# Kernel optimization log

Hardware: AMD Instinct MI355X
Metric: run time of the kernel (lower is better)

## Reference

```python
import jax, jax.numpy as jnp
import numpy as np

NEG = -1e9


def _layer_norm(x, g, b, eps=1e-5):
    m = x.mean(-1, keepdims=True)
    v = x.var(-1, keepdims=True)
    return (x - m) / jnp.sqrt(v + eps) * g + b


def _gat(x, mask, W, a):
    # x: [B,N,Fin], W: [Fin,Fout], a: [2*Fout]
    h = x @ W                                   # [B,N,Fout]
    F = W.shape[1]
    src = h @ a[:F]                             # [B,N]
    dst = h @ a[F:]                             # [B,N]
    e = jax.nn.leaky_relu(src[:, :, None] + dst[:, None, :], 0.2)  # [B,N,N]
    e = jnp.where(mask, e, NEG)
    attn = jax.nn.softmax(e, axis=-1)
    return attn @ h, attn


def _mha(x, mask, Wq, bq, Wk, bk, Wv, bv, Wo, bo, num_heads, head_dim):
    B, N, _ = x.shape
    q = (x @ Wq + bq).reshape(B, N, num_heads, head_dim)
    k = (x @ Wk + bk).reshape(B, N, num_heads, head_dim)
    v = (x @ Wv + bv).reshape(B, N, num_heads, head_dim)
    scores = jnp.einsum('bihd,bjhd->bhij', q, k) / jnp.sqrt(jnp.asarray(head_dim, x.dtype))
    scores = jnp.where(mask[:, None, :, :], scores, NEG)
    attn = jax.nn.softmax(scores, axis=-1)      # [B,H,N,N]
    ctx = jnp.einsum('bhij,bjhd->bihd', attn, v).reshape(B, N, num_heads * head_dim)
    return ctx @ Wo + bo, attn


def setup_inputs() -> dict:
    key = jax.random.key(0)
    ks = jax.random.split(key, 32)
    B, N = 64, 400
    D, Hd, E, H = 400, 256, 128, 4
    hd = Hd // H  # 64
    s = 0.02
    x = jax.random.normal(ks[0], (B, N, D), dtype=jnp.float32)
    adj = (jax.random.uniform(ks[1], (B, N, N)) < 0.15).astype(jnp.float32)
    eye = jnp.eye(N, dtype=jnp.float32)
    adj = jnp.maximum(adj, eye[None])
    def w(k, shape):
        return jax.random.normal(k, shape, dtype=jnp.float32) * s
    return {
        'x': x, 'adj': adj,
        'Wq': w(ks[2], (D, H * hd)), 'bq': jnp.zeros(H * hd),
        'Wk': w(ks[3], (D, H * hd)), 'bk': jnp.zeros(H * hd),
        'Wv': w(ks[4], (D, H * hd)), 'bv': jnp.zeros(H * hd),
        'Wo': w(ks[5], (H * hd, D)), 'bo': jnp.zeros(D),
        'gat1_W': w(ks[6], (D, Hd)), 'gat1_a': w(ks[7], (2 * Hd,)),
        'gat2_W': w(ks[8], (Hd, Hd)), 'gat2_a': w(ks[9], (2 * Hd,)),
        'gat3_W': w(ks[10], (Hd, E)), 'gat3_a': w(ks[11], (2 * E,)),
        'res1_W': w(ks[12], (D, Hd)), 'res1_b': jnp.zeros(Hd),
        'res2_W': w(ks[13], (Hd, Hd)), 'res2_b': jnp.zeros(Hd),
        'res3_W': w(ks[14], (Hd, E)), 'res3_b': jnp.zeros(E),
        'ln1_g': jnp.ones(Hd), 'ln1_b': jnp.zeros(Hd),
        'ln2_g': jnp.ones(Hd), 'ln2_b': jnp.zeros(Hd),
        'ln3_g': jnp.ones(E), 'ln3_b': jnp.zeros(E),
    }


def reference(x, adj, Wq, bq, Wk, bk, Wv, bv, Wo, bo,
              gat1_W, gat1_a, gat2_W, gat2_a, gat3_W, gat3_a,
              res1_W, res1_b, res2_W, res2_b, res3_W, res3_b,
              ln1_g, ln1_b, ln2_g, ln2_b, ln3_g, ln3_b):
    mask = adj > 0
    # eval mode: dropout is identity
    mha_out, _ = _mha(x, mask, Wq, bq, Wk, bk, Wv, bv, Wo, bo, num_heads=4, head_dim=64)
    x = x + mha_out
    g1, attn1 = _gat(x, mask, gat1_W, gat1_a)
    x = jax.nn.elu(_layer_norm(g1 + (x @ res1_W + res1_b), ln1_g, ln1_b))
    g2, attn2 = _gat(x, mask, gat2_W, gat2_a)
    x = jax.nn.elu(_layer_norm(g2 + (x @ res2_W + res2_b), ln2_g, ln2_b))
    g3, attn3 = _gat(x, mask, gat3_W, gat3_a)
    x = _layer_norm(g3 + (x @ res3_W + res3_b), ln3_g, ln3_b)
    return x, (attn1, attn2, attn3)
```

## Files before the change

### kernel.cpp

```cpp
#include <hip/hip_runtime.h>


#define NEGBIG (-1e9f)

typedef __attribute__((ext_vector_type(8))) short bf16x8;
typedef __attribute__((ext_vector_type(4))) float f32x4;

__device__ inline unsigned short f2bf(float f) {
    unsigned u = __builtin_bit_cast(unsigned, f);
    u += 0x7fffu + ((u >> 16) & 1u);
    return (unsigned short)(u >> 16);
}
__device__ inline float bf2f(unsigned short h) {
    unsigned u = ((unsigned)h) << 16;
    return __builtin_bit_cast(float, u);
}

__device__ inline float wave_max(float v) {
#pragma unroll
    for (int off = 32; off >= 1; off >>= 1)
        v = fmaxf(v, __shfl_xor(v, off, 64));
    return v;
}
__device__ inline float wave_sum(float v) {
#pragma unroll
    for (int off = 32; off >= 1; off >>= 1)
        v += __shfl_xor(v, off, 64);
    return v;
}

__global__ void build_biases(
    float* bqkv, const float* bq, const float* bk, const float* bv,
    float* bgr1, const float* r1b, float* bgr2, const float* r2b,
    float* bgr3, const float* r3b)
{
    const int t = threadIdx.x;
    bqkv[t] = bq[t]; bqkv[256 + t] = bk[t]; bqkv[512 + t] = bv[t];
    bgr1[t] = 0.f; bgr1[256 + t] = r1b[t];
    bgr2[t] = 0.f; bgr2[256 + t] = r2b[t];
    if (t < 128) { bgr3[t] = 0.f; bgr3[128 + t] = r3b[t]; }
}

__global__ __launch_bounds__(256) void transpose_to_bf16(
    const float* __restrict__ in, unsigned short* __restrict__ out,
    int R, int C, int ldIn, long sIn, long sOut)
{
    in  += (long)blockIdx.z * sIn;
    out += (long)blockIdx.z * sOut;
    __shared__ float t[32][33];
    const int r0 = blockIdx.y * 32, c0 = blockIdx.x * 32;
    const int tid = threadIdx.x;

    const int row = tid >> 3, c4 = tid & 7;
    float4 v = make_float4(0.f, 0.f, 0.f, 0.f);
    if (r0 + row < R && c0 + c4 * 4 < C)
        v = *reinterpret_cast<const float4*>(&in[(long)(r0 + row) * ldIn + c0 + c4 * 4]);
    t[row][c4 * 4 + 0] = v.x;
    t[row][c4 * 4 + 1] = v.y;
    t[row][c4 * 4 + 2] = v.z;
    t[row][c4 * 4 + 3] = v.w;
    __syncthreads();

    const int oc = tid >> 3, r4 = tid & 7;
    if (c0 + oc < C && r0 + r4 * 4 < R) {
        ushort4 o;
        o.x = f2bf(t[r4 * 4 + 0][oc]);
        o.y = f2bf(t[r4 * 4 + 1][oc]);
        o.z = f2bf(t[r4 * 4 + 2][oc]);
        o.w = f2bf(t[r4 * 4 + 3][oc]);
        *reinterpret_cast<ushort4*>(&out[(long)(c0 + oc) * R + r0 + r4 * 4]) = o;
    }
}

template<bool BIAS, bool ACCUM, bool RESID>
__global__ __launch_bounds__(512) void gemm_mfma(
    const float* __restrict__ A, const unsigned short* __restrict__ BT,
    const float* __restrict__ bias, const float* __restrict__ resid,
    float* __restrict__ C, int M, int K, int Nc, int ldA, int ldC,
    long sA, long sBT, long sC)
{
    const int bz = blockIdx.z;
    A  += (long)bz * sA;
    BT += (long)bz * sBT;
    C  += (long)bz * sC;
    const float* Rp = RESID ? (resid + (long)bz * sC) : nullptr;

    __shared__ short As[128][40];
    __shared__ short Bs[256][40];

    const int tid = threadIdx.x;
    const int lane = tid & 63, wave = tid >> 6;
    const int wm = wave >> 2, wn = wave & 3;
    const int m0 = blockIdx.y * 128, n0 = blockIdx.x * 256;

    f32x4 acc[4][4] = {};

    const int nk = (K + 31) / 32;
    for (int kt = 0; kt < nk; ++kt) {
        const int k0 = kt * 32;
        __syncthreads();
#pragma unroll
        for (int p = 0; p < 2; ++p) {
            const int idx = tid + p * 512;
            const int row = idx >> 3, k4 = idx & 7;
            const int gm = m0 + row, gk = k0 + k4 * 4;
            float4 av = make_float4(0.f, 0.f, 0.f, 0.f);
            if (gm < M && gk < K)
                av = *reinterpret_cast<const float4*>(&A[(long)gm * ldA + gk]);
            ushort4 h4;
            h4.x = f2bf(av.x); h4.y = f2bf(av.y); h4.z = f2bf(av.z); h4.w = f2bf(av.w);
            *reinterpret_cast<ushort4*>(&As[row][k4 * 4]) = h4;
        }
#pragma unroll
        for (int p = 0; p < 2; ++p) {
            const int idx = tid + p * 512;
            const int n = idx >> 2, k8 = idx & 3;
            const int gn = n0 + n, gk = k0 + k8 * 8;
            uint4 bv = make_uint4(0u, 0u, 0u, 0u);
            if (gn < Nc && gk < K)
                bv = *reinterpret_cast<const uint4*>(&BT[(long)gn * K + gk]);
            *reinterpret_cast<uint4*>(&Bs[n][k8 * 8]) = bv;
        }
        __syncthreads();

        const int fr = lane & 15, fkb = (lane >> 4) * 8;
        bf16x8 a[4], b[4];
#pragma unroll
        for (int i = 0; i < 4; ++i)
            a[i] = *reinterpret_cast<const bf16x8*>(&As[wm * 64 + i * 16 + fr][fkb]);
#pragma unroll
        for (int j = 0; j < 4; ++j)
            b[j] = *reinterpret_cast<const bf16x8*>(&Bs[wn * 64 + j * 16 + fr][fkb]);
#pragma unroll
        for (int i = 0; i < 4; ++i)
#pragma unroll
            for (int j = 0; j < 4; ++j)
                acc[i][j] = __builtin_amdgcn_mfma_f32_16x16x32_bf16(a[i], b[j], acc[i][j], 0, 0, 0);
    }

    const int fr = lane & 15, rg = lane >> 4;
#pragma unroll
    for (int i = 0; i < 4; ++i) {
#pragma unroll
        for (int j = 0; j < 4; ++j) {
#pragma unroll
            for (int r = 0; r < 4; ++r) {
                const int gm = m0 + wm * 64 + i * 16 + rg * 4 + r;
                const int gn = n0 + wn * 64 + j * 16 + fr;
                if (gm < M && gn < Nc) {
                    float v = acc[i][j][r];
                    if (BIAS)  v += bias[gn];
                    if (RESID) v += Rp[(long)gm * ldC + gn];
                    if (ACCUM) v += C[(long)gm * ldC + gn];
                    C[(long)gm * ldC + gn] = v;
                }
            }
        }
    }
}

__global__ __launch_bounds__(256) void mha_flash_mfma(
    const float* __restrict__ qkv, const float* __restrict__ adj,
    float* __restrict__ ctx, int ld)
{
    const int it = blockIdx.x, h = blockIdx.y, b = blockIdx.z;
    const int i0 = it * 64;
    const int tid = threadIdx.x;
    const int lane = tid & 63, w = tid >> 6;
    const int c = lane & 15, g = lane >> 4;

    __shared__ short Qs[64][72];
    __shared__ short Ks[64][72];
    __shared__ short Vt[64][72];
    __shared__ short Ps[64][72];
    __shared__ short Adjs[64][72];

    const long base_q = ((long)b * 400 + i0) * ld + h * 64;
#pragma unroll
    for (int p = 0; p < 4; ++p) {
        const int idx = tid + p * 256;
        const int r = idx >> 4, c4 = idx & 15;
        float4 qv = make_float4(0.f, 0.f, 0.f, 0.f);
        if (i0 + r < 400)
            qv = *reinterpret_cast<const float4*>(qkv + base_q + (long)r * ld + c4 * 4);
        ushort4 h4;
        h4.x = f2bf(qv.x); h4.y = f2bf(qv.y); h4.z = f2bf(qv.z); h4.w = f2bf(qv.w);
        *reinterpret_cast<ushort4*>(&Qs[r][c4 * 4]) = h4;
    }

    f32x4 o[4] = {};
    float m[4] = {-3e38f, -3e38f, -3e38f, -3e38f};
    float l[4] = {0.f, 0.f, 0.f, 0.f};

    for (int jt = 0; jt < 7; ++jt) {
        const int j0 = jt * 64;
        __syncthreads();

        const long base_k = ((long)b * 400 + j0) * ld + 256 + h * 64;
        const long base_v = base_k + 256;
#pragma unroll
        for (int p = 0; p < 4; ++p) {
            const int idx = tid + p * 256;
            const int r = idx >> 4, c4 = idx & 15;
            float4 kv = make_float4(0.f, 0.f, 0.f, 0.f);
            if (j0 + r < 400)
                kv = *reinterpret_cast<const float4*>(qkv + base_k + (long)r * ld + c4 * 4);
            ushort4 h4;
            h4.x = f2bf(kv.x); h4.y = f2bf(kv.y); h4.z = f2bf(kv.z); h4.w = f2bf(kv.w);
            *reinterpret_cast<ushort4*>(&Ks[r][c4 * 4]) = h4;

            float4 av = make_float4(0.f, 0.f, 0.f, 0.f);
            if (i0 + r < 400 && j0 + c4 * 4 < 400)
                av = *reinterpret_cast<const float4*>(adj + ((long)b * 400 + i0 + r) * 400 + j0 + c4 * 4);
            ushort4 mb;
            mb.x = f2bf(av.x > 0.f ? 0.f : NEGBIG);
            mb.y = f2bf(av.y > 0.f ? 0.f : NEGBIG);
            mb.z = f2bf(av.z > 0.f ? 0.f : NEGBIG);
            mb.w = f2bf(av.w > 0.f ? 0.f : NEGBIG);
            *reinterpret_cast<ushort4*>(&Adjs[r][c4 * 4]) = mb;
        }
        {
            const int j4 = tid >> 4, d4 = tid & 15;
            float vv[4][4];
#pragma unroll
            for (int t = 0; t < 4; ++t) {
                float4 vl = make_float4(0.f, 0.f, 0.f, 0.f);
                if (j0 + j4 * 4 + t < 400)
                    vl = *reinterpret_cast<const float4*>(qkv + base_v + (long)(j4 * 4 + t) * ld + d4 * 4);
                vv[t][0] = vl.x; vv[t][1] = vl.y; vv[t][2] = vl.z; vv[t][3] = vl.w;
            }
#pragma unroll
            for (int u = 0; u < 4; ++u) {
                ushort4 h4;
                h4.x = f2bf(vv[0][u]); h4.y = f2bf(vv[1][u]);
                h4.z = f2bf(vv[2][u]); h4.w = f2bf(vv[3][u]);
                *reinterpret_cast<ushort4*>(&Vt[d4 * 4 + u][j4 * 4]) = h4;
            }
        }
        __syncthreads();

        f32x4 s4[4] = {};
#pragma unroll
        for (int ks = 0; ks < 2; ++ks) {
            const bf16x8 a = *reinterpret_cast<const bf16x8*>(&Qs[w * 16 + c][ks * 32 + g * 8]);
#pragma unroll
            for (int t = 0; t < 4; ++t) {
                const bf16x8 bb = *reinterpret_cast<const bf16x8*>(&Ks[t * 16 + c][ks * 32 + g * 8]);
                s4[t] = __builtin_amdgcn_mfma_f32_16x16x32_bf16(a, bb, s4[t], 0, 0, 0);
            }
        }

        float e[4][4];
        float pmax[4];
#pragma unroll
        for (int reg = 0; reg < 4; ++reg) {
            const int qr = w * 16 + g * 4 + reg;
            float mx = -3e38f;
#pragma unroll
            for (int t = 0; t < 4; ++t) {
                const float ev = s4[t][reg] * 0.125f + bf2f((unsigned short)Adjs[qr][t * 16 + c]);
                e[t][reg] = ev;
                mx = fmaxf(mx, ev);
            }
            pmax[reg] = mx;
        }
#pragma unroll
        for (int reg = 0; reg < 4; ++reg)
#pragma unroll
            for (int off = 1; off <= 8; off <<= 1)
                pmax[reg] = fmaxf(pmax[reg], __shfl_xor(pmax[reg], off, 64));

        float al[4];
#pragma unroll
        for (int reg = 0; reg < 4; ++reg) {
            const float mn = fmaxf(m[reg], pmax[reg]);
            al[reg] = __expf(m[reg] - mn);
            m[reg] = mn;
        }

#pragma unroll
        for (int reg = 0; reg < 4; ++reg) {
            const int qr = w * 16 + g * 4 + reg;
            float psum = 0.f;
#pragma unroll
            for (int t = 0; t < 4; ++t) {
                const float p = __expf(e[t][reg] - m[reg]);
                psum += p;
                Ps[qr][t * 16 + c] = (short)f2bf(p);
            }
            l[reg] = l[reg] * al[reg] + psum;
        }

#pragma unroll
        for (int dt = 0; dt < 4; ++dt)
#pragma unroll
            for (int reg = 0; reg < 4; ++reg)
                o[dt][reg] *= al[reg];

#pragma unroll
        for (int ks = 0; ks < 2; ++ks) {
            const bf16x8 a = *reinterpret_cast<const bf16x8*>(&Ps[w * 16 + c][ks * 32 + g * 8]);
#pragma unroll
            for (int dt = 0; dt < 4; ++dt) {
                const bf16x8 bb = *reinterpret_cast<const bf16x8*>(&Vt[dt * 16 + c][ks * 32 + g * 8]);
                o[dt] = __builtin_amdgcn_mfma_f32_16x16x32_bf16(a, bb, o[dt], 0, 0, 0);
            }
        }
    }

#pragma unroll
    for (int reg = 0; reg < 4; ++reg)
#pragma unroll
        for (int off = 1; off <= 8; off <<= 1)
            l[reg] += __shfl_xor(l[reg], off, 64);

#pragma unroll
    for (int reg = 0; reg < 4; ++reg) {
        const int gi = i0 + w * 16 + g * 4 + reg;
        if (gi < 400) {
            const float inv = 1.f / l[reg];
#pragma unroll
            for (int dt = 0; dt < 4; ++dt)
                ctx[((long)b * 400 + gi) * 256 + h * 64 + dt * 16 + c] = o[dt][reg] * inv;
        }
    }
}

__global__ __launch_bounds__(256) void gat_srcdst(
    const float* __restrict__ h, const float* __restrict__ a,
    float* __restrict__ src, float* __restrict__ dst, int F, int ld)
{
    const int row = blockIdx.x * 4 + (threadIdx.x >> 6);
    const int lane = threadIdx.x & 63;
    const float* hp = h + (long)row * ld;
    float s = 0.f, d = 0.f;
    for (int f = lane; f < F; f += 64) {
        const float hv = hp[f];
        s += hv * a[f];
        d += hv * a[F + f];
    }
    s = wave_sum(s);
    d = wave_sum(d);
    if (lane == 0) { src[row] = s; dst[row] = d; }
}

__global__ __launch_bounds__(256) void gat_attn(
    const float* __restrict__ src, const float* __restrict__ dst,
    const float* __restrict__ adj, float* __restrict__ attn)
{
    const int row = blockIdx.x * 4 + (threadIdx.x >> 6);
    const int b = row / 400;
    const int lane = threadIdx.x & 63;
    const float si = src[row];
    const float* db = dst + (long)b * 400;
    const float* adjrow = adj + (long)row * 400;

    float e[7];
    float mx = -3.0e38f;
#pragma unroll
    for (int t = 0; t < 7; ++t) {
        const int j = lane + 64 * t;
        float v = -3.0e38f;
        if (j < 400) {
            v = si + db[j];
            v = (v > 0.f) ? v : 0.2f * v;
            if (!(adjrow[j] > 0.f)) v = NEGBIG;
        }
        e[t] = v;
        mx = fmaxf(mx, v);
    }
    mx = wave_max(mx);

    float p[7];
    float sum = 0.f;
#pragma unroll
    for (int t = 0; t < 7; ++t) {
        const int j = lane + 64 * t;
        if (j < 400) {
            p[t] = __expf(e[t] - mx);
            sum += p[t];
        }
    }
    sum = wave_sum(sum);
    const float inv = 1.f / sum;
#pragma unroll
    for (int t = 0; t < 7; ++t) {
        const int j = lane + 64 * t;
        if (j < 400) attn[(long)row * 400 + j] = p[t] * inv;
    }
}

template<int F, bool ELU>
__global__ __launch_bounds__(256) void ln_kernel(
    const float* __restrict__ in, int ldIn, const float* __restrict__ g,
    const float* __restrict__ b, float* __restrict__ out)
{
    const int row = blockIdx.x * 4 + (threadIdx.x >> 6);
    const int lane = threadIdx.x & 63;
    constexpr int PER = F / 64;
    const float* ip = in + (long)row * ldIn;

    float v[PER];
    float s = 0.f;
#pragma unroll
    for (int t = 0; t < PER; ++t) {
        v[t] = ip[lane + 64 * t];
        s += v[t];
    }
    s = wave_sum(s);
    const float mean = s * (1.f / F);
    float vs = 0.f;
#pragma unroll
    for (int t = 0; t < PER; ++t) {
        const float d = v[t] - mean;
        vs += d * d;
    }
    vs = wave_sum(vs);
    const float rstd = rsqrtf(vs * (1.f / F) + 1e-5f);
#pragma unroll
    for (int t = 0; t < PER; ++t) {
        const int col = lane + 64 * t;
        float y = (v[t] - mean) * rstd * g[col] + b[col];
        if (ELU) y = (y > 0.f) ? y : expm1f(y);
        out[(long)row * F + col] = y;
    }
}

extern "C" void kernel_launch(void* const* d_in, const int* in_sizes, int n_in,
                              void* d_out, int out_size, void* d_ws, size_t ws_size,
                              hipStream_t stream) {
    const float* x    = (const float*)d_in[0];
    const float* adj  = (const float*)d_in[1];
    const float* Wq   = (const float*)d_in[2];
    const float* bq   = (const float*)d_in[3];
    const float* Wk   = (const float*)d_in[4];
    const float* bk   = (const float*)d_in[5];
    const float* Wv   = (const float*)d_in[6];
    const float* bv   = (const float*)d_in[7];
    const float* Wo   = (const float*)d_in[8];
    const float* bo   = (const float*)d_in[9];
    const float* g1W  = (const float*)d_in[10];
    const float* g1a  = (const float*)d_in[11];
    const float* g2W  = (const float*)d_in[12];
    const float* g2a  = (const float*)d_in[13];
    const float* g3W  = (const float*)d_in[14];
    const float* g3a  = (const float*)d_in[15];
    const float* r1W  = (const float*)d_in[16];
    const float* r1b  = (const float*)d_in[17];
    const float* r2W  = (const float*)d_in[18];
    const float* r2b  = (const float*)d_in[19];
    const float* r3W  = (const float*)d_in[20];
    const float* r3b  = (const float*)d_in[21];
    const float* ln1g = (const float*)d_in[22];
    const float* ln1b = (const float*)d_in[23];
    const float* ln2g = (const float*)d_in[24];
    const float* ln2b = (const float*)d_in[25];
    const float* ln3g = (const float*)d_in[26];
    const float* ln3b = (const float*)d_in[27];

    float* out_x = (float*)d_out;
    float* attn1 = out_x + 3276800;
    float* attn2 = attn1 + 10240000;
    float* attn3 = attn2 + 10240000;

    float* bufA = (float*)d_ws;
    float* bufB = bufA + 6553600;
    float* bufC = bufB + 6553600;
    float* bufD = bufC + 6553600;
    float* srcb = bufD + 6553600;
    float* dstb = srcb + 25600;
    unsigned short* wT   = (unsigned short*)(dstb + 25600);
    unsigned short* wTq  = wT;
    unsigned short* wTk  = wT + 102400;
    unsigned short* wTv  = wT + 204800;
    unsigned short* wTo  = wT + 307200;
    unsigned short* wTg1 = wT + 409600;
    unsigned short* wTr1 = wT + 512000;
    unsigned short* wTg2 = wT + 614400;
    unsigned short* wTr2 = wT + 679936;
    unsigned short* wTg3 = wT + 745472;
    unsigned short* wTr3 = wT + 778240;
    float* bias0 = (float*)(wT + 811008);
    float* bqkv = bias0;
    float* bgr1 = bqkv + 768;
    float* bgr2 = bgr1 + 512;
    float* bgr3 = bgr2 + 512;

    float* qkv = bufA;
    float* ctx = bufD;
    float* xc  = attn1;
    float* hr1 = bufA;
    float* hr3 = bufA;
    unsigned short* hT = (unsigned short*)bufD;
    float* x2 = bufC;
    float* x3 = bufC;

    const dim3 b256(256), b512(512);
    const int M = 25600;

    build_biases<<<1, b256, 0, stream>>>(bqkv, bq, bk, bv, bgr1, r1b, bgr2, r2b, bgr3, r3b);
    transpose_to_bf16<<<dim3(8, 13), b256, 0, stream>>>(Wq,  wTq, 400, 256, 256, 0, 0);
    transpose_to_bf16<<<dim3(8, 13), b256, 0, stream>>>(Wk,  wTk, 400, 256, 256, 0, 0);
    transpose_to_bf16<<<dim3(8, 13), b256, 0, stream>>>(Wv,  wTv, 400, 256, 256, 0, 0);
    transpose_to_bf16<<<dim3(13, 8), b256, 0, stream>>>(Wo,  wTo, 256, 400, 400, 0, 0);
    transpose_to_bf16<<<dim3(8, 13), b256, 0, stream>>>(g1W, wTg1, 400, 256, 256, 0, 0);
    transpose_to_bf16<<<dim3(8, 13), b256, 0, stream>>>(r1W, wTr1, 400, 256, 256, 0, 0);
    transpose_to_bf16<<<dim3(8, 8),  b256, 0, stream>>>(g2W, wTg2, 256, 256, 256, 0, 0);
    transpose_to_bf16<<<dim3(8, 8),  b256, 0, stream>>>(r2W, wTr2, 256, 256, 256, 0, 0);
    transpose_to_bf16<<<dim3(4, 8),  b256, 0, stream>>>(g3W, wTg3, 256, 128, 128, 0, 0);
    transpose_to_bf16<<<dim3(4, 8),  b256, 0, stream>>>(r3W, wTr3, 256, 128, 128, 0, 0);

    gemm_mfma<true, false, false><<<dim3(3, 200), b512, 0, stream>>>(
        x, wTq, bqkv, nullptr, qkv, M, 400, 768, 400, 768, 0, 0, 0);
    mha_flash_mfma<<<dim3(7, 4, 64), b256, 0, stream>>>(qkv, adj, ctx, 768);
    gemm_mfma<true, false, true><<<dim3(2, 200), b512, 0, stream>>>(
        ctx, wTo, bo, x, xc, M, 256, 400, 256, 400, 0, 0, 0);

    gemm_mfma<true, false, false><<<dim3(2, 200), b512, 0, stream>>>(
        xc, wTg1, bgr1, nullptr, hr1, M, 400, 512, 400, 512, 0, 0, 0);
    gat_srcdst<<<dim3(6400), b256, 0, stream>>>(hr1, g1a, srcb, dstb, 256, 512);
    gat_attn<<<dim3(6400), b256, 0, stream>>>(srcb, dstb, adj, attn1);
    transpose_to_bf16<<<dim3(8, 13, 64), b256, 0, stream>>>(hr1, hT, 400, 256, 512, 204800, 102400);
    gemm_mfma<false, true, false><<<dim3(1, 4, 64), b512, 0, stream>>>(
        attn1, hT, nullptr, nullptr, hr1 + 256, 400, 400, 256, 400, 512, 160000, 102400, 204800);
    ln_kernel<256, true><<<dim3(6400), b256, 0, stream>>>(hr1 + 256, 512, ln1g, ln1b, x2);

    gemm_mfma<true, false, false><<<dim3(2, 200), b512, 0, stream>>>(
        x2, wTg2, bgr2, nullptr, hr1, M, 256, 512, 256, 512, 0, 0, 0);
    gat_srcdst<<<dim3(6400), b256, 0, stream>>>(hr1, g2a, srcb, dstb, 256, 512);
    gat_attn<<<dim3(6400), b256, 0, stream>>>(srcb, dstb, adj, attn2);
    transpose_to_bf16<<<dim3(8, 13, 64), b256, 0, stream>>>(hr1, hT, 400, 256, 512, 204800, 102400);
    gemm_mfma<false, true, false><<<dim3(1, 4, 64), b512, 0, stream>>>(
        attn2, hT, nullptr, nullptr, hr1 + 256, 400, 400, 256, 400, 512, 160000, 102400, 204800);
    ln_kernel<256, true><<<dim3(6400), b256, 0, stream>>>(hr1 + 256, 512, ln2g, ln2b, x3);

    gemm_mfma<true, false, false><<<dim3(1, 200), b512, 0, stream>>>(
        x3, wTg3, bgr3, nullptr, hr3, M, 256, 256, 256, 256, 0, 0, 0);
    gat_srcdst<<<dim3(6400), b256, 0, stream>>>(hr3, g3a, srcb, dstb, 128, 256);
    gat_attn<<<dim3(6400), b256, 0, stream>>>(srcb, dstb, adj, attn3);
    transpose_to_bf16<<<dim3(4, 13, 64), b256, 0, stream>>>(hr3, hT, 400, 128, 256, 102400, 51200);
    gemm_mfma<false, true, false><<<dim3(1, 4, 64), b512, 0, stream>>>(
        attn3, hT, nullptr, nullptr, hr3 + 128, 400, 400, 128, 400, 256, 160000, 51200, 102400);
    ln_kernel<128, false><<<dim3(6400), b256, 0, stream>>>(hr3 + 128, 256, ln3g, ln3b, out_x);
}
```

Before: 852.3 us.

## Keep inter-stage activations in bf16 and precompute a bf16 additive mask

QKV, the attention context, the post-MHA residual stream, the GAT layer inputs and a copy of each GAT attention matrix are now stored in bf16 instead of fp32. The GEMM kernel gains template paths to load bf16 A tiles directly and to write bf16 outputs. The fp32 adjacency is converted once into a bf16 additive mask (0 or -1e9), which the MHA and GAT attention kernels read instead of re-reading and comparing the fp32 adjacency each time. This is meant to cut global memory traffic and in-kernel conversion work. The costs are an extra bf16 attention write per GAT layer and lower precision for the residual stream and intermediate activations.

```diff
diff --git a/kernel.cpp b/kernel.cpp
--- a/kernel.cpp
+++ b/kernel.cpp
@@ -16,16 +16,16 @@
     return __builtin_bit_cast(float, u);
 }
 
+__device__ inline float wave_sum(float v) {
+#pragma unroll
+    for (int off = 32; off >= 1; off >>= 1)
+        v += __shfl_xor(v, off, 64);
+    return v;
+}
 __device__ inline float wave_max(float v) {
 #pragma unroll
     for (int off = 32; off >= 1; off >>= 1)
         v = fmaxf(v, __shfl_xor(v, off, 64));
-    return v;
-}
-__device__ inline float wave_sum(float v) {
-#pragma unroll
-    for (int off = 32; off >= 1; off >>= 1)
-        v += __shfl_xor(v, off, 64);
     return v;
 }
 
@@ -39,6 +39,19 @@
     bgr1[t] = 0.f; bgr1[256 + t] = r1b[t];
     bgr2[t] = 0.f; bgr2[256 + t] = r2b[t];
     if (t < 128) { bgr3[t] = 0.f; bgr3[128 + t] = r3b[t]; }
+}
+
+__global__ __launch_bounds__(256) void adj2mask(
+    const float* __restrict__ adj, unsigned short* __restrict__ mb)
+{
+    const long i = ((long)blockIdx.x * 256 + threadIdx.x) * 4;
+    const float4 a = *reinterpret_cast<const float4*>(adj + i);
+    ushort4 o;
+    o.x = f2bf(a.x > 0.f ? 0.f : NEGBIG);
+    o.y = f2bf(a.y > 0.f ? 0.f : NEGBIG);
+    o.z = f2bf(a.z > 0.f ? 0.f : NEGBIG);
+    o.w = f2bf(a.w > 0.f ? 0.f : NEGBIG);
+    *reinterpret_cast<ushort4*>(mb + i) = o;
 }
 
 __global__ __launch_bounds__(256) void transpose_to_bf16(
@@ -72,17 +85,19 @@
     }
 }
 
-template<bool BIAS, bool ACCUM, bool RESID>
+template<bool BIAS, bool ACCUM, bool RESID, bool ABHALF, bool OUTBF16>
 __global__ __launch_bounds__(512) void gemm_mfma(
-    const float* __restrict__ A, const unsigned short* __restrict__ BT,
+    const void* __restrict__ Av, const unsigned short* __restrict__ BT,
     const float* __restrict__ bias, const float* __restrict__ resid,
-    float* __restrict__ C, int M, int K, int Nc, int ldA, int ldC,
+    void* __restrict__ Cv, int M, int K, int Nc, int ldA, int ldC,
     long sA, long sBT, long sC)
 {
     const int bz = blockIdx.z;
-    A  += (long)bz * sA;
+    const float* Af = ABHALF ? nullptr : ((const float*)Av + (long)bz * sA);
+    const unsigned short* Ah = ABHALF ? ((const unsigned short*)Av + (long)bz * sA) : nullptr;
     BT += (long)bz * sBT;
-    C  += (long)bz * sC;
+    float* Cf = OUTBF16 ? nullptr : ((float*)Cv + (long)bz * sC);
+    unsigned short* Ch = OUTBF16 ? ((unsigned short*)Cv + (long)bz * sC) : nullptr;
     const float* Rp = RESID ? (resid + (long)bz * sC) : nullptr;
 
     __shared__ short As[128][40];
@@ -99,17 +114,26 @@
     for (int kt = 0; kt < nk; ++kt) {
         const int k0 = kt * 32;
         __syncthreads();
-#pragma unroll
-        for (int p = 0; p < 2; ++p) {
-            const int idx = tid + p * 512;
-            const int row = idx >> 3, k4 = idx & 7;
-            const int gm = m0 + row, gk = k0 + k4 * 4;
-            float4 av = make_float4(0.f, 0.f, 0.f, 0.f);
+        if (ABHALF) {
+            const int row = tid >> 2, k8 = tid & 3;
+            const int gm = m0 + row, gk = k0 + k8 * 8;
+            uint4 av = make_uint4(0u, 0u, 0u, 0u);
             if (gm < M && gk < K)
-                av = *reinterpret_cast<const float4*>(&A[(long)gm * ldA + gk]);
-            ushort4 h4;
-            h4.x = f2bf(av.x); h4.y = f2bf(av.y); h4.z = f2bf(av.z); h4.w = f2bf(av.w);
-            *reinterpret_cast<ushort4*>(&As[row][k4 * 4]) = h4;
+                av = *reinterpret_cast<const uint4*>(&Ah[(long)gm * ldA + gk]);
+            *reinterpret_cast<uint4*>(&As[row][k8 * 8]) = av;
+        } else {
+#pragma unroll
+            for (int p = 0; p < 2; ++p) {
+                const int idx = tid + p * 512;
+                const int row = idx >> 3, k4 = idx & 7;
+                const int gm = m0 + row, gk = k0 + k4 * 4;
+                float4 av = make_float4(0.f, 0.f, 0.f, 0.f);
+                if (gm < M && gk < K)
+                    av = *reinterpret_cast<const float4*>(&Af[(long)gm * ldA + gk]);
+                ushort4 h4;
+                h4.x = f2bf(av.x); h4.y = f2bf(av.y); h4.z = f2bf(av.z); h4.w = f2bf(av.w);
+                *reinterpret_cast<ushort4*>(&As[row][k4 * 4]) = h4;
+            }
         }
 #pragma unroll
         for (int p = 0; p < 2; ++p) {
@@ -151,8 +175,12 @@
                     float v = acc[i][j][r];
                     if (BIAS)  v += bias[gn];
                     if (RESID) v += Rp[(long)gm * ldC + gn];
-                    if (ACCUM) v += C[(long)gm * ldC + gn];
-                    C[(long)gm * ldC + gn] = v;
+                    if (OUTBF16) {
+                        Ch[(long)gm * ldC + gn] = f2bf(v);
+                    } else {
+                        if (ACCUM) v += Cf[(long)gm * ldC + gn];
+                        Cf[(long)gm * ldC + gn] = v;
+                    }
                 }
             }
         }
@@ -160,14 +188,15 @@
 }
 
 __global__ __launch_bounds__(256) void mha_flash_mfma(
-    const float* __restrict__ qkv, const float* __restrict__ adj,
-    float* __restrict__ ctx, int ld)
+    const unsigned short* __restrict__ qkv, const unsigned short* __restrict__ mask,
+    unsigned short* __restrict__ ctx, int ld)
 {
     const int it = blockIdx.x, h = blockIdx.y, b = blockIdx.z;
     const int i0 = it * 64;
     const int tid = threadIdx.x;
     const int lane = tid & 63, w = tid >> 6;
     const int c = lane & 15, g = lane >> 4;
+    const unsigned short NEGBF = f2bf(NEGBIG);
 
     __shared__ short Qs[64][72];
     __shared__ short Ks[64][72];
@@ -177,15 +206,13 @@
 
     const long base_q = ((long)b * 400 + i0) * ld + h * 64;
 #pragma unroll
-    for (int p = 0; p < 4; ++p) {
+    for (int p = 0; p < 2; ++p) {
         const int idx = tid + p * 256;
-        const int r = idx >> 4, c4 = idx & 15;
-        float4 qv = make_float4(0.f, 0.f, 0.f, 0.f);
+        const int r = idx >> 3, c8 = idx & 7;
+        uint4 qv = make_uint4(0u, 0u, 0u, 0u);
         if (i0 + r < 400)
-            qv = *reinterpret_cast<const float4*>(qkv + base_q + (long)r * ld + c4 * 4);
-        ushort4 h4;
-        h4.x = f2bf(qv.x); h4.y = f2bf(qv.y); h4.z = f2bf(qv.z); h4.w = f2bf(qv.w);
-        *reinterpret_cast<ushort4*>(&Qs[r][c4 * 4]) = h4;
+            qv = *reinterpret_cast<const uint4*>(qkv + base_q + (long)r * ld + c8 * 8);
+        *reinterpret_cast<uint4*>(&Qs[r][c8 * 8]) = qv;
     }
 
     f32x4 o[4] = {};
@@ -199,41 +226,41 @@
         const long base_k = ((long)b * 400 + j0) * ld + 256 + h * 64;
         const long base_v = base_k + 256;
 #pragma unroll
-        for (int p = 0; p < 4; ++p) {
+        for (int p = 0; p < 2; ++p) {
             const int idx = tid + p * 256;
-            const int r = idx >> 4, c4 = idx & 15;
-            float4 kv = make_float4(0.f, 0.f, 0.f, 0.f);
+            const int r = idx >> 3, c8 = idx & 7;
+            uint4 kv = make_uint4(0u, 0u, 0u, 0u);
             if (j0 + r < 400)
-                kv = *reinterpret_cast<const float4*>(qkv + base_k + (long)r * ld + c4 * 4);
-            ushort4 h4;
-            h4.x = f2bf(kv.x); h4.y = f2bf(kv.y); h4.z = f2bf(kv.z); h4.w = f2bf(kv.w);
-            *reinterpret_cast<ushort4*>(&Ks[r][c4 * 4]) = h4;
-
-            float4 av = make_float4(0.f, 0.f, 0.f, 0.f);
-            if (i0 + r < 400 && j0 + c4 * 4 < 400)
-                av = *reinterpret_cast<const float4*>(adj + ((long)b * 400 + i0 + r) * 400 + j0 + c4 * 4);
-            ushort4 mb;
-            mb.x = f2bf(av.x > 0.f ? 0.f : NEGBIG);
-            mb.y = f2bf(av.y > 0.f ? 0.f : NEGBIG);
-            mb.z = f2bf(av.z > 0.f ? 0.f : NEGBIG);
-            mb.w = f2bf(av.w > 0.f ? 0.f : NEGBIG);
-            *reinterpret_cast<ushort4*>(&Adjs[r][c4 * 4]) = mb;
+                kv = *reinterpret_cast<const uint4*>(qkv + base_k + (long)r * ld + c8 * 8);
+            *reinterpret_cast<uint4*>(&Ks[r][c8 * 8]) = kv;
+
+            ushort4 mb = make_ushort4(NEGBF, NEGBF, NEGBF, NEGBF);
+            ushort4 mb2 = mb;
+            if (i0 + r < 400 && j0 + c8 * 8 + 7 < 400) {
+                const uint4 mv = *reinterpret_cast<const uint4*>(
+                    mask + ((long)b * 400 + i0 + r) * 400 + j0 + c8 * 8);
+                mb  = *reinterpret_cast<const ushort4*>(&mv.x);
+                mb2 = *reinterpret_cast<const ushort4*>(&mv.z);
+            }
+            *reinterpret_cast<ushort4*>(&Adjs[r][c8 * 8]) = mb;
+            *reinterpret_cast<ushort4*>(&Adjs[r][c8 * 8 + 4]) = mb2;
         }
         {
             const int j4 = tid >> 4, d4 = tid & 15;
-            float vv[4][4];
+            ushort4 vl[4];
 #pragma unroll
             for (int t = 0; t < 4; ++t) {
-                float4 vl = make_float4(0.f, 0.f, 0.f, 0.f);
+                vl[t] = make_ushort4(0, 0, 0, 0);
                 if (j0 + j4 * 4 + t < 400)
-                    vl = *reinterpret_cast<const float4*>(qkv + base_v + (long)(j4 * 4 + t) * ld + d4 * 4);
-                vv[t][0] = vl.x; vv[t][1] = vl.y; vv[t][2] = vl.z; vv[t][3] = vl.w;
+                    vl[t] = *reinterpret_cast<const ushort4*>(qkv + base_v + (long)(j4 * 4 + t) * ld + d4 * 4);
             }
 #pragma unroll
             for (int u = 0; u < 4; ++u) {
                 ushort4 h4;
-                h4.x = f2bf(vv[0][u]); h4.y = f2bf(vv[1][u]);
-                h4.z = f2bf(vv[2][u]); h4.w = f2bf(vv[3][u]);
+                h4.x = ((const unsigned short*)&vl[0])[u];
+                h4.y = ((const unsigned short*)&vl[1])[u];
+                h4.z = ((const unsigned short*)&vl[2])[u];
+                h4.w = ((const unsigned short*)&vl[3])[u];
                 *reinterpret_cast<ushort4*>(&Vt[d4 * 4 + u][j4 * 4]) = h4;
             }
         }
@@ -321,7 +348,7 @@
             const float inv = 1.f / l[reg];
 #pragma unroll
             for (int dt = 0; dt < 4; ++dt)
-                ctx[((long)b * 400 + gi) * 256 + h * 64 + dt * 16 + c] = o[dt][reg] * inv;
+                ctx[((long)b * 400 + gi) * 256 + h * 64 + dt * 16 + c] = f2bf(o[dt][reg] * inv);
         }
     }
 }
@@ -346,14 +373,15 @@
 
 __global__ __launch_bounds__(256) void gat_attn(
     const float* __restrict__ src, const float* __restrict__ dst,
-    const float* __restrict__ adj, float* __restrict__ attn)
+    const unsigned short* __restrict__ mask,
+    float* __restrict__ attn, unsigned short* __restrict__ attnb)
 {
     const int row = blockIdx.x * 4 + (threadIdx.x >> 6);
     const int b = row / 400;
     const int lane = threadIdx.x & 63;
     const float si = src[row];
     const float* db = dst + (long)b * 400;
-    const float* adjrow = adj + (long)row * 400;
+    const unsigned short* mrow = mask + (long)row * 400;
 
     float e[7];
     float mx = -3.0e38f;
@@ -364,7 +392,7 @@
         if (j < 400) {
             v = si + db[j];
             v = (v > 0.f) ? v : 0.2f * v;
-            if (!(adjrow[j] > 0.f)) v = NEGBIG;
+            v += bf2f(mrow[j]);
         }
         e[t] = v;
         mx = fmaxf(mx, v);
@@ -386,14 +414,18 @@
 #pragma unroll
     for (int t = 0; t < 7; ++t) {
         const int j = lane + 64 * t;
-        if (j < 400) attn[(long)row * 400 + j] = p[t] * inv;
-    }
-}
-
-template<int F, bool ELU>
+        if (j < 400) {
+            const float pv = p[t] * inv;
+            attn[(long)row * 400 + j] = pv;
+            attnb[(long)row * 400 + j] = f2bf(pv);
+        }
+    }
+}
+
+template<int F, bool ELU, bool OB16>
 __global__ __launch_bounds__(256) void ln_kernel(
     const float* __restrict__ in, int ldIn, const float* __restrict__ g,
-    const float* __restrict__ b, float* __restrict__ out)
+    const float* __restrict__ b, void* __restrict__ outv)
 {
     const int row = blockIdx.x * 4 + (threadIdx.x >> 6);
     const int lane = threadIdx.x & 63;
@@ -422,7 +454,8 @@
         const int col = lane + 64 * t;
         float y = (v[t] - mean) * rstd * g[col] + b[col];
         if (ELU) y = (y > 0.f) ? y : expm1f(y);
-        out[(long)row * F + col] = y;
+        if (OB16) ((unsigned short*)outv)[(long)row * F + col] = f2bf(y);
+        else      ((float*)outv)[(long)row * F + col] = y;
     }
 }
 
@@ -463,13 +496,17 @@
     float* attn2 = attn1 + 10240000;
     float* attn3 = attn2 + 10240000;
 
-    float* bufA = (float*)d_ws;
-    float* bufB = bufA + 6553600;
-    float* bufC = bufB + 6553600;
-    float* bufD = bufC + 6553600;
-    float* srcb = bufD + 6553600;
-    float* dstb = srcb + 25600;
-    unsigned short* wT   = (unsigned short*)(dstb + 25600);
+    char* wsb = (char*)d_ws;
+    float*          hrF  = (float*)wsb;
+    unsigned short* ctxH = (unsigned short*)wsb;
+    unsigned short* qkvH  = (unsigned short*)(wsb + 52428800);
+    unsigned short* attnH = qkvH;
+    unsigned short* x2H   = qkvH;
+    unsigned short* hT    = (unsigned short*)(wsb + 72908800);
+    unsigned short* maskH = (unsigned short*)(wsb + 91750400);
+    float* srcb = (float*)(wsb + 112230400);
+    float* dstb = (float*)(wsb + 112332800);
+    unsigned short* wT = (unsigned short*)(wsb + 112435200);
     unsigned short* wTq  = wT;
     unsigned short* wTk  = wT + 102400;
     unsigned short* wTv  = wT + 204800;
@@ -480,25 +517,17 @@
     unsigned short* wTr2 = wT + 679936;
     unsigned short* wTg3 = wT + 745472;
     unsigned short* wTr3 = wT + 778240;
-    float* bias0 = (float*)(wT + 811008);
-    float* bqkv = bias0;
+    float* bqkv = (float*)(wsb + 114057216);
     float* bgr1 = bqkv + 768;
     float* bgr2 = bgr1 + 512;
     float* bgr3 = bgr2 + 512;
-
-    float* qkv = bufA;
-    float* ctx = bufD;
-    float* xc  = attn1;
-    float* hr1 = bufA;
-    float* hr3 = bufA;
-    unsigned short* hT = (unsigned short*)bufD;
-    float* x2 = bufC;
-    float* x3 = bufC;
+    unsigned short* xcH = (unsigned short*)attn1;
 
     const dim3 b256(256), b512(512);
     const int M = 25600;
 
     build_biases<<<1, b256, 0, stream>>>(bqkv, bq, bk, bv, bgr1, r1b, bgr2, r2b, bgr3, r3b);
+    adj2mask<<<dim3(10000), b256, 0, stream>>>(adj, maskH);
     transpose_to_bf16<<<dim3(8, 13), b256, 0, stream>>>(Wq,  wTq, 400, 256, 256, 0, 0);
     transpose_to_bf16<<<dim3(8, 13), b256, 0, stream>>>(Wk,  wTk, 400, 256, 256, 0, 0);
     transpose_to_bf16<<<dim3(8, 13), b256, 0, stream>>>(Wv,  wTv, 400, 256, 256, 0, 0);
@@ -510,36 +539,36 @@
     transpose_to_bf16<<<dim3(4, 8),  b256, 0, stream>>>(g3W, wTg3, 256, 128, 128, 0, 0);
     transpose_to_bf16<<<dim3(4, 8),  b256, 0, stream>>>(r3W, wTr3, 256, 128, 128, 0, 0);
 
-    gemm_mfma<true, false, false><<<dim3(3, 200), b512, 0, stream>>>(
-        x, wTq, bqkv, nullptr, qkv, M, 400, 768, 400, 768, 0, 0, 0);
-    mha_flash_mfma<<<dim3(7, 4, 64), b256, 0, stream>>>(qkv, adj, ctx, 768);
-    gemm_mfma<true, false, true><<<dim3(2, 200), b512, 0, stream>>>(
-        ctx, wTo, bo, x, xc, M, 256, 400, 256, 400, 0, 0, 0);
-
-    gemm_mfma<true, false, false><<<dim3(2, 200), b512, 0, stream>>>(
-        xc, wTg1, bgr1, nullptr, hr1, M, 400, 512, 400, 512, 0, 0, 0);
-    gat_srcdst<<<dim3(6400), b256, 0, stream>>>(hr1, g1a, srcb, dstb, 256, 512);
-    gat_attn<<<dim3(6400), b256, 0, stream>>>(srcb, dstb, adj, attn1);
-    transpose_to_bf16<<<dim3(8, 13, 64), b256, 0, stream>>>(hr1, hT, 400, 256, 512, 204800, 102400);
-    gemm_mfma<false, true, false><<<dim3(1, 4, 64), b512, 0, stream>>>(
-        attn1, hT, nullptr, nullptr, hr1 + 256, 400, 400, 256, 400, 512, 160000, 102400, 204800);
-    ln_kernel<256, true><<<dim3(6400), b256, 0, stream>>>(hr1 + 256, 512, ln1g, ln1b, x2);
-
-    gemm_mfma<true, false, false><<<dim3(2, 200), b512, 0, stream>>>(
-        x2, wTg2, bgr2, nullptr, hr1, M, 256, 512, 256, 512, 0, 0, 0);
-    gat_srcdst<<<dim3(6400), b256, 0, stream>>>(hr1, g2a, srcb, dstb, 256, 512);
-    gat_attn<<<dim3(6400), b256, 0, stream>>>(srcb, dstb, adj, attn2);
-    transpose_to_bf16<<<dim3(8, 13, 64), b256, 0, stream>>>(hr1, hT, 400, 256, 512, 204800, 102400);
-    gemm_mfma<false, true, false><<<dim3(1, 4, 64), b512, 0, stream>>>(
-        attn2, hT, nullptr, nullptr, hr1 + 256, 400, 400, 256, 400, 512, 160000, 102400, 204800);
-    ln_kernel<256, true><<<dim3(6400), b256, 0, stream>>>(hr1 + 256, 512, ln2g, ln2b, x3);
-
-    gemm_mfma<true, false, false><<<dim3(1, 200), b512, 0, stream>>>(
-        x3, wTg3, bgr3, nullptr, hr3, M, 256, 256, 256, 256, 0, 0, 0);
-    gat_srcdst<<<dim3(6400), b256, 0, stream>>>(hr3, g3a, srcb, dstb, 128, 256);
-    gat_attn<<<dim3(6400), b256, 0, stream>>>(srcb, dstb, adj, attn3);
-    transpose_to_bf16<<<dim3(4, 13, 64), b256, 0, stream>>>(hr3, hT, 400, 128, 256, 102400, 51200);
-    gemm_mfma<false, true, false><<<dim3(1, 4, 64), b512, 0, stream>>>(
-        attn3, hT, nullptr, nullptr, hr3 + 128, 400, 400, 128, 400, 256, 160000, 51200, 102400);
-    ln_kernel<128, false><<<dim3(6400), b256, 0, stream>>>(hr3 + 128, 256, ln3g, ln3b, out_x);
-}
+    gemm_mfma<true, false, false, false, true><<<dim3(3, 200), b512, 0, stream>>>(
+        x, wTq, bqkv, nullptr, qkvH, M, 400, 768, 400, 768, 0, 0, 0);
+    mha_flash_mfma<<<dim3(7, 4, 64), b256, 0, stream>>>(qkvH, maskH, ctxH, 768);
+    gemm_mfma<true, false, true, true, true><<<dim3(2, 200), b512, 0, stream>>>(
+        ctxH, wTo, bo, x, xcH, M, 256, 400, 256, 400, 0, 0, 0);
+
+    gemm_mfma<true, false, false, true, false><<<dim3(2, 200), b512, 0, stream>>>(
+        xcH, wTg1, bgr1, nullptr, hrF, M, 400, 512, 400, 512, 0, 0, 0);
+    gat_srcdst<<<dim3(6400), b256, 0, stream>>>(hrF, g1a, srcb, dstb, 256, 512);
+    gat_attn<<<dim3(6400), b256, 0, stream>>>(srcb, dstb, maskH, attn1, attnH);
+    transpose_to_bf16<<<dim3(8, 13, 64), b256, 0, stream>>>(hrF, hT, 400, 256, 512, 204800, 102400);
+    gemm_mfma<false, true, false, true, false><<<dim3(1, 4, 64), b512, 0, stream>>>(
+        attnH, hT, nullptr, nullptr, hrF + 256, 400, 400, 256, 400, 512, 160000, 102400, 204800);
+    ln_kernel<256, true, true><<<dim3(6400), b256, 0, stream>>>(hrF + 256, 512, ln1g, ln1b, x2H);
+
+    gemm_mfma<true, false, false, true, false><<<dim3(2, 200), b512, 0, stream>>>(
+        x2H, wTg2, bgr2, nullptr, hrF, M, 256, 512, 256, 512, 0, 0, 0);
+    gat_srcdst<<<dim3(6400), b256, 0, stream>>>(hrF, g2a, srcb, dstb, 256, 512);
+    gat_attn<<<dim3(6400), b256, 0, stream>>>(srcb, dstb, maskH, attn2, attnH);
+    transpose_to_bf16<<<dim3(8, 13, 64), b256, 0, stream>>>(hrF, hT, 400, 256, 512, 204800, 102400);
+    gemm_mfma<false, true, false, true, false><<<dim3(1, 4, 64), b512, 0, stream>>>(
+        attnH, hT, nullptr, nullptr, hrF + 256, 400, 400, 256, 400, 512, 160000, 102400, 204800);
+    ln_kernel<256, true, true><<<dim3(6400), b256, 0, stream>>>(hrF + 256, 512, ln2g, ln2b, x2H);
+
+    gemm_mfma<true, false, false, true, false><<<dim3(1, 200), b512, 0, stream>>>(
+        x2H, wTg3, bgr3, nullptr, hrF, M, 256, 256, 256, 256, 0, 0, 0);
+    gat_srcdst<<<dim3(6400), b256, 0, stream>>>(hrF, g3a, srcb, dstb, 128, 256);
+    gat_attn<<<dim3(6400), b256, 0, stream>>>(srcb, dstb, maskH, attn3, attnH);
+    transpose_to_bf16<<<dim3(4, 13, 64), b256, 0, stream>>>(hrF, hT, 400, 128, 256, 102400, 51200);
+    gemm_mfma<false, true, false, true, false><<<dim3(1, 4, 64), b512, 0, stream>>>(
+        attnH, hT, nullptr, nullptr, hrF + 128, 400, 400, 128, 400, 256, 160000, 51200, 102400);
+    ln_kernel<128, false, false><<<dim3(6400), b256, 0, stream>>>(hrF + 128, 256, ln3g, ln3b, out_x);
+}
```

New measurement: 760.6 us. -10.8%, faster.
